# Optimization experiments

Measured on AMD Instinct MI355X. Metric: run time of the kernel, lower is better.

Reference implementation:

```python
import jax, jax.numpy as jnp
import numpy as np

B, S, E, H = 1, 2048, 1024, 16
D = E // H  # head_dim = 64


def setup_inputs() -> dict:
    key = jax.random.key(0)
    ks = jax.random.split(key, 9)
    sd = 0.02
    hidden_states = jax.random.normal(ks[0], (B, S, E), dtype=jnp.float32)
    # causal mask: positions with mask==0 are filled with -inf (per masked_fill_)
    mask = jnp.tril(jnp.ones((1, 1, S, S), dtype=bool))
    Wq = jax.random.normal(ks[1], (E, E), dtype=jnp.float32) * sd
    bq = jax.random.normal(ks[2], (E,), dtype=jnp.float32) * sd
    Wk = jax.random.normal(ks[3], (D, E), dtype=jnp.float32) * sd
    bk = jax.random.normal(ks[4], (D,), dtype=jnp.float32) * sd
    Wv = jax.random.normal(ks[5], (D, E), dtype=jnp.float32) * sd
    bv = jax.random.normal(ks[6], (D,), dtype=jnp.float32) * sd
    Wo = jax.random.normal(ks[7], (E, E), dtype=jnp.float32) * sd
    bo = jax.random.normal(ks[8], (E,), dtype=jnp.float32) * sd
    return {"hidden_states": hidden_states, "mask": mask,
            "Wq": Wq, "bq": bq, "Wk": Wk, "bk": bk,
            "Wv": Wv, "bv": bv, "Wo": Wo, "bo": bo}


def reference(hidden_states, mask, Wq, bq, Wk, bk, Wv, bv, Wo, bo):
    bsz, tgt_len, embed_dim = hidden_states.shape
    # projections (torch Linear: x @ W^T + b)
    q = hidden_states @ Wq.T + bq                       # [B, S, E]
    q = q.reshape(bsz, tgt_len, H, D).transpose(0, 2, 1, 3)  # [B, H, S, D]
    k = hidden_states @ Wk.T + bk                       # [B, S, D] shared single KV head
    v = hidden_states @ Wv.T + bv                       # [B, S, D]
    scaling = jnp.sqrt(jnp.asarray(D, dtype=hidden_states.dtype))
    # QK^T with implicit broadcast of the shared K head (instead of expand)
    scores = jnp.einsum('bhqd,bkd->bhqk', q, k) / scaling   # [B, H, S, S]
    scores = jnp.where(mask, scores, -jnp.inf)
    probs = jax.nn.softmax(scores, axis=-1)             # dropout p=0 -> identity
    attn = jnp.einsum('bhqk,bkd->bhqd', probs, v)       # [B, H, S, D]
    attn = attn.transpose(0, 2, 1, 3).reshape(bsz, tgt_len, H * D)
    return attn @ Wo.T + bo                             # [B, S, E]
```

## Files before the change

### kernel.cpp

```cpp
#include <hip/hip_runtime.h>
#include <hip/hip_bf16.h>

typedef __hip_bfloat16 bf16;
typedef __attribute__((ext_vector_type(8))) short short8;
typedef __attribute__((ext_vector_type(4))) short short4v;
typedef __attribute__((ext_vector_type(4))) float f32x4;

__device__ __forceinline__ short8 ld8(const void* p) { return *(const short8*)p; }
__device__ __forceinline__ short4v ld4(const void* p) { return *(const short4v*)p; }

__device__ __forceinline__ void async_cp16(bf16* lds, const bf16* g) {
    __builtin_amdgcn_global_load_lds(
        (const __attribute__((address_space(1))) unsigned int*)g,
        (__attribute__((address_space(3))) unsigned int*)lds, 16, 0, 0);
}

struct bf4 { bf16 a, b, c, d; };

__global__ void cast_kernel(const float* __restrict__ s0, bf16* __restrict__ d0, int n0_,
                            const float* __restrict__ s1, bf16* __restrict__ d1, int n1_,
                            const float* __restrict__ s2, bf16* __restrict__ d2, int n2_,
                            const float* __restrict__ s3, bf16* __restrict__ d3, int n3_,
                            const float* __restrict__ s4, bf16* __restrict__ d4, int n4_) {
    const float* srcs[5] = {s0, s1, s2, s3, s4};
    bf16* dsts[5] = {d0, d1, d2, d3, d4};
    int ns[5] = {n0_, n1_, n2_, n3_, n4_};
    int stride = gridDim.x * blockDim.x;
    int t0 = blockIdx.x * blockDim.x + threadIdx.x;
#pragma unroll
    for (int a = 0; a < 5; ++a) {
        const float4* src = (const float4*)srcs[a];
        bf4* dst = (bf4*)dsts[a];
        int n4 = ns[a] >> 2;
        for (int i = t0; i < n4; i += stride) {
            float4 v = src[i];
            bf4 o = {__float2bfloat16(v.x), __float2bfloat16(v.y),
                     __float2bfloat16(v.z), __float2bfloat16(v.w)};
            dst[i] = o;
        }
    }
}

#define GEMM_STAGE(dst, src_base, row0, ldk)                                   \
    _Pragma("unroll")                                                          \
    for (int u = 0; u < 4; ++u) {                                              \
        int t = wave * 4 + u;                                                  \
        int row = t * 4 + (lane >> 4);                                         \
        int gsrc = (lane & 15) ^ (row & 15);                                   \
        async_cp16(&dst[t * 4][0], src_base + (size_t)(row0 + row) * ldk + k0 + gsrc * 8); \
    }

__global__ void qkv_proj_kernel(const bf16* __restrict__ A,
                                const bf16* __restrict__ Wq, const bf16* __restrict__ Wk,
                                const bf16* __restrict__ Wv,
                                const float* __restrict__ bq, const float* __restrict__ bk,
                                const float* __restrict__ bv,
                                bf16* __restrict__ qo, bf16* __restrict__ ko,
                                bf16* __restrict__ vto, int M, int K) {
    __shared__ __align__(16) bf16 As[64][128];
    __shared__ __align__(16) bf16 Bs[64][128];
    const int nt = blockIdx.x;
    const bf16* W;
    const float* bias;
    int mode, nw0;
    if (nt < 16)      { W = Wq; bias = bq; mode = 0; nw0 = nt * 64; }
    else if (nt == 16){ W = Wk; bias = bk; mode = 1; nw0 = 0; }
    else              { W = Wv; bias = bv; mode = 2; nw0 = 0; }

    const int tid = threadIdx.x;
    const int wave = tid >> 6, lane = tid & 63;
    const int l16 = lane & 15, quad = lane >> 4;
    const int wr = wave >> 1, wc = wave & 1;
    const int m0 = blockIdx.y * 64;

    f32x4 acc[2][2];
    const f32x4 z = {0.f, 0.f, 0.f, 0.f};
#pragma unroll
    for (int mi = 0; mi < 2; ++mi)
#pragma unroll
        for (int ni = 0; ni < 2; ++ni) acc[mi][ni] = z;

    for (int k0 = 0; k0 < K; k0 += 128) {
        GEMM_STAGE(As, A, m0, K)
        GEMM_STAGE(Bs, W, nw0, K)
        __syncthreads();

        short8 af[2][4], bfr[2][4];
#pragma unroll
        for (int mi = 0; mi < 2; ++mi) {
            int R = wr * 32 + mi * 16 + l16;
#pragma unroll
            for (int kc = 0; kc < 4; ++kc)
                af[mi][kc] = ld8(&As[R][((kc * 4 + quad) ^ (R & 15)) * 8]);
        }
#pragma unroll
        for (int ni = 0; ni < 2; ++ni) {
            int r = wc * 32 + ni * 16 + l16;
#pragma unroll
            for (int kc = 0; kc < 4; ++kc)
                bfr[ni][kc] = ld8(&Bs[r][((kc * 4 + quad) ^ (r & 15)) * 8]);
        }
#pragma unroll
        for (int kc = 0; kc < 4; ++kc)
#pragma unroll
            for (int mi = 0; mi < 2; ++mi)
#pragma unroll
                for (int ni = 0; ni < 2; ++ni)
                    acc[mi][ni] = __builtin_amdgcn_mfma_f32_16x16x32_bf16(
                        af[mi][kc], bfr[ni][kc], acc[mi][ni], 0, 0, 0);
        __syncthreads();
    }

#pragma unroll
    for (int mi = 0; mi < 2; ++mi)
#pragma unroll
        for (int ni = 0; ni < 2; ++ni)
#pragma unroll
            for (int r = 0; r < 4; ++r) {
                int row = m0 + wr * 32 + mi * 16 + quad * 4 + r;
                int c = wc * 32 + ni * 16 + l16;
                float v = acc[mi][ni][r] + bias[nw0 + c];
                if (mode == 0)
                    qo[(size_t)row * 1024 + nt * 64 + c] = __float2bfloat16(v * 0.125f);
                else if (mode == 1)
                    ko[(size_t)row * 64 + c] = __float2bfloat16(v);
                else
                    vto[(size_t)c * M + row] = __float2bfloat16(v);
            }
}

__global__ void gemm_bt_mfma(const bf16* __restrict__ A, const bf16* __restrict__ W,
                             const float* __restrict__ bias, float* __restrict__ C,
                             int M, int N, int K) {
    __shared__ __align__(16) bf16 As[64][128];
    __shared__ __align__(16) bf16 Bs[64][128];
    const int tid = threadIdx.x;
    const int wave = tid >> 6, lane = tid & 63;
    const int l16 = lane & 15, quad = lane >> 4;
    const int wr = wave >> 1, wc = wave & 1;
    const int m0 = blockIdx.y * 64, n0 = blockIdx.x * 64;

    f32x4 acc[2][2];
    const f32x4 z = {0.f, 0.f, 0.f, 0.f};
#pragma unroll
    for (int mi = 0; mi < 2; ++mi)
#pragma unroll
        for (int ni = 0; ni < 2; ++ni) acc[mi][ni] = z;

    for (int k0 = 0; k0 < K; k0 += 128) {
        GEMM_STAGE(As, A, m0, K)
        GEMM_STAGE(Bs, W, n0, K)
        __syncthreads();

        short8 af[2][4], bfr[2][4];
#pragma unroll
        for (int mi = 0; mi < 2; ++mi) {
            int R = wr * 32 + mi * 16 + l16;
#pragma unroll
            for (int kc = 0; kc < 4; ++kc)
                af[mi][kc] = ld8(&As[R][((kc * 4 + quad) ^ (R & 15)) * 8]);
        }
#pragma unroll
        for (int ni = 0; ni < 2; ++ni) {
            int r = wc * 32 + ni * 16 + l16;
#pragma unroll
            for (int kc = 0; kc < 4; ++kc)
                bfr[ni][kc] = ld8(&Bs[r][((kc * 4 + quad) ^ (r & 15)) * 8]);
        }
#pragma unroll
        for (int kc = 0; kc < 4; ++kc)
#pragma unroll
            for (int mi = 0; mi < 2; ++mi)
#pragma unroll
                for (int ni = 0; ni < 2; ++ni)
                    acc[mi][ni] = __builtin_amdgcn_mfma_f32_16x16x32_bf16(
                        af[mi][kc], bfr[ni][kc], acc[mi][ni], 0, 0, 0);
        __syncthreads();
    }

#pragma unroll
    for (int mi = 0; mi < 2; ++mi)
#pragma unroll
        for (int ni = 0; ni < 2; ++ni)
#pragma unroll
            for (int r = 0; r < 4; ++r) {
                int row = m0 + wr * 32 + mi * 16 + quad * 4 + r;
                int col = n0 + wc * 32 + ni * 16 + l16;
                C[(size_t)row * N + col] = acc[mi][ni][r] + bias[col];
            }
}

__global__ void flash_mfma_kernel(const bf16* __restrict__ Q, const bf16* __restrict__ Kg,
                                  const bf16* __restrict__ VT,
                                  bf16* __restrict__ Opart, float* __restrict__ Lpart,
                                  bf16* __restrict__ attn, int S) {
    const int s = blockIdx.x;
    int i, c;
    if (s < 32)      { c = 0; i = s; }
    else if (s < 56) { c = 1; i = s - 24; }
    else if (s < 72) { c = 2; i = s - 40; }
    else             { c = 3; i = s - 48; }

    __shared__ __align__(16) bf16 Ks[64][64];
    __shared__ __align__(16) bf16 Vt[64][64];

    const int h = blockIdx.y;
    const int q0 = i * 64;
    const int tid = threadIdx.x;
    const int wave = tid >> 6, lane = tid & 63;
    const int l16 = lane & 15, quad = lane >> 4;
    const int lr = lane >> 3, lsw = (lane & 7) ^ (lr & 7);
    const int qrow = q0 + wave * 16;

    short8 qf[2];
#pragma unroll
    for (int kc = 0; kc < 2; ++kc)
        qf[kc] = ld8(Q + (size_t)(qrow + l16) * 1024 + h * 64 + kc * 32 + quad * 8);

    f32x4 of[4];
    const f32x4 z = {0.f, 0.f, 0.f, 0.f};
#pragma unroll
    for (int dt = 0; dt < 4; ++dt) of[dt] = z;
    float lsum = 0.f;

    const int jt0 = c * 8;
    const int jt1 = min(c * 8 + 8, i + 1);

    for (int jt = jt0; jt < jt1; ++jt) {
        const int j0 = jt * 64;
#pragma unroll
        for (int u = 0; u < 2; ++u) {
            int t = wave * 2 + u;
            async_cp16(&Ks[t * 8][0], Kg + (size_t)(j0 + t * 8 + lr) * 64 + lsw * 8);
            async_cp16(&Vt[t * 8][0], VT + (size_t)(t * 8 + lr) * S + j0 + lsw * 8);
        }
        __syncthreads();

        f32x4 sc[4];
#pragma unroll
        for (int nt = 0; nt < 4; ++nt) {
            int R = nt * 16 + l16;
            sc[nt] = __builtin_amdgcn_mfma_f32_16x16x32_bf16(
                ld8(&Ks[R][(quad ^ (R & 7)) * 8]), qf[0], z, 0, 0, 0);
            sc[nt] = __builtin_amdgcn_mfma_f32_16x16x32_bf16(
                ld8(&Ks[R][((4 + quad) ^ (R & 7)) * 8]), qf[1], sc[nt], 0, 0, 0);
        }
        if (j0 + 63 > qrow) {
#pragma unroll
            for (int nt = 0; nt < 4; ++nt)
#pragma unroll
                for (int r = 0; r < 4; ++r)
                    if (j0 + nt * 16 + quad * 4 + r > qrow + l16) sc[nt][r] = -1e30f;
        }

        short4v p4[4];
#pragma unroll
        for (int nt = 0; nt < 4; ++nt)
#pragma unroll
            for (int r = 0; r < 4; ++r) {
                bf16 b = __float2bfloat16(__expf(sc[nt][r]));
                lsum += __bfloat162float(b);
                p4[nt][r] = *reinterpret_cast<short*>(&b);
            }

#pragma unroll
        for (int dt = 0; dt < 4; ++dt) {
            int d = dt * 16 + l16;
            int xr = d & 7;
#pragma unroll
            for (int nt = 0; nt < 4; ++nt) {
                int g = 2 * nt + (quad >> 1);
                short4v vf = ld4(&Vt[d][((g ^ xr) * 8) + (quad & 1) * 4]);
                of[dt] = __builtin_amdgcn_mfma_f32_16x16x16bf16_1k(
                    p4[nt], vf, of[dt], 0, 0, 0);
            }
        }
        __syncthreads();
    }

    float Lred = lsum;
    Lred += __shfl_xor(Lred, 16);
    Lred += __shfl_xor(Lred, 32);

    if (s < 8) {
        float inv[4];
#pragma unroll
        for (int r = 0; r < 4; ++r)
            inv[r] = 1.f / __shfl(Lred, quad * 4 + r);
#pragma unroll
        for (int dt = 0; dt < 4; ++dt)
#pragma unroll
            for (int r = 0; r < 4; ++r) {
                int row = q0 + wave * 16 + quad * 4 + r;
                attn[(size_t)row * 1024 + h * 64 + dt * 16 + l16] =
                    __float2bfloat16(of[dt][r] * inv[r]);
            }
        return;
    }

    bf16* Op = Opart + ((size_t)s * 16 + h) * 4096;
#pragma unroll
    for (int dt = 0; dt < 4; ++dt)
#pragma unroll
        for (int r = 0; r < 4; ++r) {
            int row = wave * 16 + quad * 4 + r;
            Op[row * 64 + dt * 16 + l16] = __float2bfloat16(of[dt][r]);
        }
    if (quad == 0) {
        float* L = Lpart + ((size_t)s * 16 + h) * 64;
        L[wave * 16 + l16] = Lred;
    }
}

__global__ void flash_merge_kernel(const bf16* __restrict__ Opart,
                                   const float* __restrict__ Lpart,
                                   bf16* __restrict__ attn) {
    const int i = blockIdx.x + 8, h = blockIdx.y;
    const int nch = (i >> 3) + 1;
    const int tid = threadIdx.x;
    const int row = tid >> 2, cg = (tid & 3) * 16;

    float L = 0.f;
    for (int cc = 0; cc < nch; ++cc) {
        int s = (cc == 0) ? i : (cc == 1) ? 24 + i : (cc == 2) ? 40 + i : 48 + i;
        L += Lpart[((size_t)s * 16 + h) * 64 + row];
    }
    float inv = 1.f / L;

    float o[16];
#pragma unroll
    for (int j = 0; j < 16; ++j) o[j] = 0.f;
    for (int cc = 0; cc < nch; ++cc) {
        int s = (cc == 0) ? i : (cc == 1) ? 24 + i : (cc == 2) ? 40 + i : 48 + i;
        const bf16* Op = Opart + ((size_t)s * 16 + h) * 4096 + row * 64 + cg;
#pragma unroll
        for (int j = 0; j < 16; ++j) o[j] += __bfloat162float(Op[j]);
    }
    bf16* dst = attn + (size_t)(i * 64 + row) * 1024 + h * 64 + cg;
#pragma unroll
    for (int j = 0; j < 16; ++j) dst[j] = __float2bfloat16(o[j] * inv);
}

extern "C" void kernel_launch(void* const* d_in, const int* in_sizes, int n_in,
                              void* d_out, int out_size, void* d_ws, size_t ws_size,
                              hipStream_t stream) {
    const int S = 2048, E = 1024, D = 64;

    const float* hs = (const float*)d_in[0];
    const float* Wq = (const float*)d_in[2];
    const float* bq = (const float*)d_in[3];
    const float* Wk = (const float*)d_in[4];
    const float* bk = (const float*)d_in[5];
    const float* Wv = (const float*)d_in[6];
    const float* bv = (const float*)d_in[7];
    const float* Wo = (const float*)d_in[8];
    const float* bo = (const float*)d_in[9];
    float* out = (float*)d_out;

    bf16* ws = (bf16*)d_ws;
    bf16* hsb = ws;
    bf16* wqb = hsb + (size_t)S * E;
    bf16* wkb = wqb + (size_t)E * E;
    bf16* wvb = wkb + (size_t)D * E;
    bf16* wob = wvb + (size_t)D * E;
    bf16* q = wob + (size_t)E * E;
    bf16* kbuf = q + (size_t)S * E;
    bf16* vt = kbuf + (size_t)S * D;
    bf16* attn = vt + (size_t)S * D;
    bf16* Opart = attn + (size_t)S * E;
    float* Lpart = (float*)(Opart + (size_t)1280 * 4096);

    cast_kernel<<<512, 256, 0, stream>>>(hs, hsb, S * E,
                                         Wq, wqb, E * E,
                                         Wk, wkb, D * E,
                                         Wv, wvb, D * E,
                                         Wo, wob, E * E);
    qkv_proj_kernel<<<dim3(18, S / 64), 256, 0, stream>>>(hsb, wqb, wkb, wvb,
                                                          bq, bk, bv,
                                                          q, kbuf, vt, S, E);
    flash_mfma_kernel<<<dim3(80, 16), 256, 0, stream>>>(q, kbuf, vt, Opart, Lpart, attn, S);
    flash_merge_kernel<<<dim3(24, 16), 256, 0, stream>>>(Opart, Lpart, attn);
    gemm_bt_mfma<<<dim3(E / 64, S / 64), 256, 0, stream>>>(attn, wob, bo, out, S, E, E);
}
```

Before: 138.8 us.

## Split flash attention waves over key columns with register-prefetched K/V

The flash kernel now gives each wave 16 key columns of every 64-key tile instead of 16 query rows. K and V fragments are loaded straight into registers with a one-tile-ahead prefetch, which removes the per-tile LDS staging and the two barriers per iteration. Each wave then keeps partial outputs for all 64 query rows, and these are reduced across waves through LDS atomicAdds into an fp32 scratch buffer before the existing output and partial-write paths. This raises register pressure (launch bounds set to 3 blocks per CU) and adds an LDS atomic reduction at the end of every block.

Measured after the change: 265.3 us. +91.2%, slower.

```diff
diff --git a/kernel.cpp b/kernel.cpp
--- a/kernel.cpp
+++ b/kernel.cpp
@@ -190,10 +190,11 @@
             }
 }
 
-__global__ void flash_mfma_kernel(const bf16* __restrict__ Q, const bf16* __restrict__ Kg,
-                                  const bf16* __restrict__ VT,
-                                  bf16* __restrict__ Opart, float* __restrict__ Lpart,
-                                  bf16* __restrict__ attn, int S) {
+__global__ void __launch_bounds__(256, 3)
+flash_mfma_kernel(const bf16* __restrict__ Q, const bf16* __restrict__ Kg,
+                  const bf16* __restrict__ VT,
+                  bf16* __restrict__ Opart, float* __restrict__ Lpart,
+                  bf16* __restrict__ attn, int S) {
     const int s = blockIdx.x;
     int i, c;
     if (s < 32)      { c = 0; i = s; }
@@ -201,115 +202,128 @@
     else if (s < 72) { c = 2; i = s - 40; }
     else             { c = 3; i = s - 48; }
 
-    __shared__ __align__(16) bf16 Ks[64][64];
-    __shared__ __align__(16) bf16 Vt[64][64];
+    __shared__ float Osum[64][68];
+    __shared__ float Ls[64];
 
     const int h = blockIdx.y;
     const int q0 = i * 64;
     const int tid = threadIdx.x;
-    const int wave = tid >> 6, lane = tid & 63;
+    const int wk = tid >> 6, lane = tid & 63;
     const int l16 = lane & 15, quad = lane >> 4;
-    const int lr = lane >> 3, lsw = (lane & 7) ^ (lr & 7);
-    const int qrow = q0 + wave * 16;
-
-    short8 qf[2];
-#pragma unroll
-    for (int kc = 0; kc < 2; ++kc)
-        qf[kc] = ld8(Q + (size_t)(qrow + l16) * 1024 + h * 64 + kc * 32 + quad * 8);
-
-    f32x4 of[4];
+
+    for (int j = tid; j < 64 * 68; j += 256) (&Osum[0][0])[j] = 0.f;
+    if (tid < 64) Ls[tid] = 0.f;
+
+    short8 qfr[4][2];
+#pragma unroll
+    for (int qt = 0; qt < 4; ++qt)
+#pragma unroll
+        for (int dc = 0; dc < 2; ++dc)
+            qfr[qt][dc] = ld8(Q + (size_t)(q0 + qt * 16 + l16) * 1024 + h * 64
+                                + dc * 32 + quad * 8);
+
+    f32x4 of[4][4];
     const f32x4 z = {0.f, 0.f, 0.f, 0.f};
 #pragma unroll
-    for (int dt = 0; dt < 4; ++dt) of[dt] = z;
-    float lsum = 0.f;
+    for (int qt = 0; qt < 4; ++qt)
+#pragma unroll
+        for (int dt = 0; dt < 4; ++dt) of[qt][dt] = z;
+    float lsum[4] = {0.f, 0.f, 0.f, 0.f};
 
     const int jt0 = c * 8;
     const int jt1 = min(c * 8 + 8, i + 1);
 
+    const bf16* kbase = Kg + (size_t)(wk * 16 + l16) * 64 + quad * 8;
+    const bf16* vbase = VT + (size_t)l16 * S + wk * 16 + quad * 4;
+
+    short8  kc0 = ld8(kbase + (size_t)jt0 * 4096);
+    short8  kc1 = ld8(kbase + (size_t)jt0 * 4096 + 32);
+    short4v vc0 = ld4(vbase + jt0 * 64);
+    short4v vc1 = ld4(vbase + (size_t)16 * S + jt0 * 64);
+    short4v vc2 = ld4(vbase + (size_t)32 * S + jt0 * 64);
+    short4v vc3 = ld4(vbase + (size_t)48 * S + jt0 * 64);
+
     for (int jt = jt0; jt < jt1; ++jt) {
         const int j0 = jt * 64;
-#pragma unroll
-        for (int u = 0; u < 2; ++u) {
-            int t = wave * 2 + u;
-            async_cp16(&Ks[t * 8][0], Kg + (size_t)(j0 + t * 8 + lr) * 64 + lsw * 8);
-            async_cp16(&Vt[t * 8][0], VT + (size_t)(t * 8 + lr) * S + j0 + lsw * 8);
-        }
-        __syncthreads();
+        const bool more = (jt + 1 < jt1);
+        short8 kn0, kn1; short4v vn0, vn1, vn2, vn3;
+        if (more) {
+            kn0 = ld8(kbase + (size_t)(jt + 1) * 4096);
+            kn1 = ld8(kbase + (size_t)(jt + 1) * 4096 + 32);
+            vn0 = ld4(vbase + (jt + 1) * 64);
+            vn1 = ld4(vbase + (size_t)16 * S + (jt + 1) * 64);
+            vn2 = ld4(vbase + (size_t)32 * S + (jt + 1) * 64);
+            vn3 = ld4(vbase + (size_t)48 * S + (jt + 1) * 64);
+        }
 
         f32x4 sc[4];
 #pragma unroll
-        for (int nt = 0; nt < 4; ++nt) {
-            int R = nt * 16 + l16;
-            sc[nt] = __builtin_amdgcn_mfma_f32_16x16x32_bf16(
-                ld8(&Ks[R][(quad ^ (R & 7)) * 8]), qf[0], z, 0, 0, 0);
-            sc[nt] = __builtin_amdgcn_mfma_f32_16x16x32_bf16(
-                ld8(&Ks[R][((4 + quad) ^ (R & 7)) * 8]), qf[1], sc[nt], 0, 0, 0);
-        }
-        if (j0 + 63 > qrow) {
-#pragma unroll
-            for (int nt = 0; nt < 4; ++nt)
+        for (int qt = 0; qt < 4; ++qt) {
+            sc[qt] = __builtin_amdgcn_mfma_f32_16x16x32_bf16(kc0, qfr[qt][0], z, 0, 0, 0);
+            sc[qt] = __builtin_amdgcn_mfma_f32_16x16x32_bf16(kc1, qfr[qt][1], sc[qt], 0, 0, 0);
+        }
+
+        const int kg = j0 + wk * 16 + quad * 4;
+#pragma unroll
+        for (int qt = 0; qt < 4; ++qt) {
+            if (j0 + wk * 16 + 15 > q0 + qt * 16) {
 #pragma unroll
                 for (int r = 0; r < 4; ++r)
-                    if (j0 + nt * 16 + quad * 4 + r > qrow + l16) sc[nt][r] = -1e30f;
+                    if (kg + r > q0 + qt * 16 + l16) sc[qt][r] = -1e30f;
+            }
         }
 
         short4v p4[4];
 #pragma unroll
-        for (int nt = 0; nt < 4; ++nt)
+        for (int qt = 0; qt < 4; ++qt)
 #pragma unroll
             for (int r = 0; r < 4; ++r) {
-                bf16 b = __float2bfloat16(__expf(sc[nt][r]));
-                lsum += __bfloat162float(b);
-                p4[nt][r] = *reinterpret_cast<short*>(&b);
+                bf16 b = __float2bfloat16(__expf(sc[qt][r]));
+                lsum[qt] += __bfloat162float(b);
+                p4[qt][r] = *reinterpret_cast<short*>(&b);
             }
 
 #pragma unroll
-        for (int dt = 0; dt < 4; ++dt) {
-            int d = dt * 16 + l16;
-            int xr = d & 7;
-#pragma unroll
-            for (int nt = 0; nt < 4; ++nt) {
-                int g = 2 * nt + (quad >> 1);
-                short4v vf = ld4(&Vt[d][((g ^ xr) * 8) + (quad & 1) * 4]);
-                of[dt] = __builtin_amdgcn_mfma_f32_16x16x16bf16_1k(
-                    p4[nt], vf, of[dt], 0, 0, 0);
-            }
-        }
-        __syncthreads();
-    }
-
-    float Lred = lsum;
-    Lred += __shfl_xor(Lred, 16);
-    Lred += __shfl_xor(Lred, 32);
-
+        for (int qt = 0; qt < 4; ++qt) {
+            of[qt][0] = __builtin_amdgcn_mfma_f32_16x16x16bf16_1k(p4[qt], vc0, of[qt][0], 0, 0, 0);
+            of[qt][1] = __builtin_amdgcn_mfma_f32_16x16x16bf16_1k(p4[qt], vc1, of[qt][1], 0, 0, 0);
+            of[qt][2] = __builtin_amdgcn_mfma_f32_16x16x16bf16_1k(p4[qt], vc2, of[qt][2], 0, 0, 0);
+            of[qt][3] = __builtin_amdgcn_mfma_f32_16x16x16bf16_1k(p4[qt], vc3, of[qt][3], 0, 0, 0);
+        }
+
+        if (more) { kc0 = kn0; kc1 = kn1; vc0 = vn0; vc1 = vn1; vc2 = vn2; vc3 = vn3; }
+    }
+
+    __syncthreads();
+
+#pragma unroll
+    for (int qt = 0; qt < 4; ++qt)
+#pragma unroll
+        for (int dt = 0; dt < 4; ++dt)
+#pragma unroll
+            for (int r = 0; r < 4; ++r)
+                atomicAdd(&Osum[qt * 16 + quad * 4 + r][dt * 16 + l16], of[qt][dt][r]);
+#pragma unroll
+    for (int qt = 0; qt < 4; ++qt)
+        atomicAdd(&Ls[qt * 16 + l16], lsum[qt]);
+    __syncthreads();
+
+    const int row = tid >> 2, cg = (tid & 3) * 16;
     if (s < 8) {
-        float inv[4];
-#pragma unroll
-        for (int r = 0; r < 4; ++r)
-            inv[r] = 1.f / __shfl(Lred, quad * 4 + r);
-#pragma unroll
-        for (int dt = 0; dt < 4; ++dt)
-#pragma unroll
-            for (int r = 0; r < 4; ++r) {
-                int row = q0 + wave * 16 + quad * 4 + r;
-                attn[(size_t)row * 1024 + h * 64 + dt * 16 + l16] =
-                    __float2bfloat16(of[dt][r] * inv[r]);
-            }
+        float inv = 1.f / Ls[row];
+        bf16* dst = attn + (size_t)(q0 + row) * 1024 + h * 64 + cg;
+#pragma unroll
+        for (int j = 0; j < 16; ++j)
+            dst[j] = __float2bfloat16(Osum[row][cg + j] * inv);
         return;
     }
 
-    bf16* Op = Opart + ((size_t)s * 16 + h) * 4096;
-#pragma unroll
-    for (int dt = 0; dt < 4; ++dt)
-#pragma unroll
-        for (int r = 0; r < 4; ++r) {
-            int row = wave * 16 + quad * 4 + r;
-            Op[row * 64 + dt * 16 + l16] = __float2bfloat16(of[dt][r]);
-        }
-    if (quad == 0) {
-        float* L = Lpart + ((size_t)s * 16 + h) * 64;
-        L[wave * 16 + l16] = Lred;
-    }
+    bf16* Op = Opart + ((size_t)s * 16 + h) * 4096 + row * 64 + cg;
+#pragma unroll
+    for (int j = 0; j < 16; ++j)
+        Op[j] = __float2bfloat16(Osum[row][cg + j]);
+    if ((tid & 3) == 0)
+        Lpart[((size_t)s * 16 + h) * 64 + row] = Ls[row];
 }
 
 __global__ void flash_merge_kernel(const bf16* __restrict__ Opart,
```

## Process two query heads per block to reuse shared K/V tiles

Applied to the files above, without the earlier changes.

Each flash-attention block now handles two heads at once. It loads the shared single-head K and V tiles into LDS and registers once, then runs both heads' QK^T, softmax and PV MFMAs from them. This halves the grid and the redundant K/V global and LDS traffic for the multi-query layout. In exchange, per-thread register use grows (two accumulator sets, cached K/V fragments), which is capped with launch bounds, and fewer blocks means less parallelism.

New measurement: 145.3 us. +4.7%, slower.

```diff
diff --git a/kernel.cpp b/kernel.cpp
--- a/kernel.cpp
+++ b/kernel.cpp
@@ -190,10 +190,11 @@
             }
 }
 
-__global__ void flash_mfma_kernel(const bf16* __restrict__ Q, const bf16* __restrict__ Kg,
-                                  const bf16* __restrict__ VT,
-                                  bf16* __restrict__ Opart, float* __restrict__ Lpart,
-                                  bf16* __restrict__ attn, int S) {
+__global__ void __launch_bounds__(256, 2)
+flash_mfma_kernel(const bf16* __restrict__ Q, const bf16* __restrict__ Kg,
+                  const bf16* __restrict__ VT,
+                  bf16* __restrict__ Opart, float* __restrict__ Lpart,
+                  bf16* __restrict__ attn, int S) {
     const int s = blockIdx.x;
     int i, c;
     if (s < 32)      { c = 0; i = s; }
@@ -204,7 +205,7 @@
     __shared__ __align__(16) bf16 Ks[64][64];
     __shared__ __align__(16) bf16 Vt[64][64];
 
-    const int h = blockIdx.y;
+    const int h0 = blockIdx.y * 2;
     const int q0 = i * 64;
     const int tid = threadIdx.x;
     const int wave = tid >> 6, lane = tid & 63;
@@ -212,16 +213,21 @@
     const int lr = lane >> 3, lsw = (lane & 7) ^ (lr & 7);
     const int qrow = q0 + wave * 16;
 
-    short8 qf[2];
-#pragma unroll
-    for (int kc = 0; kc < 2; ++kc)
-        qf[kc] = ld8(Q + (size_t)(qrow + l16) * 1024 + h * 64 + kc * 32 + quad * 8);
-
-    f32x4 of[4];
+    short8 qf[2][2];
+#pragma unroll
+    for (int hh = 0; hh < 2; ++hh)
+#pragma unroll
+        for (int kc = 0; kc < 2; ++kc)
+            qf[hh][kc] = ld8(Q + (size_t)(qrow + l16) * 1024 + (h0 + hh) * 64
+                               + kc * 32 + quad * 8);
+
+    f32x4 of[2][4];
     const f32x4 z = {0.f, 0.f, 0.f, 0.f};
 #pragma unroll
-    for (int dt = 0; dt < 4; ++dt) of[dt] = z;
-    float lsum = 0.f;
+    for (int hh = 0; hh < 2; ++hh)
+#pragma unroll
+        for (int dt = 0; dt < 4; ++dt) of[hh][dt] = z;
+    float lsum[2] = {0.f, 0.f};
 
     const int jt0 = c * 8;
     const int jt1 = min(c * 8 + 8, i + 1);
@@ -236,33 +242,14 @@
         }
         __syncthreads();
 
-        f32x4 sc[4];
+        short8 kf[4][2];
 #pragma unroll
         for (int nt = 0; nt < 4; ++nt) {
             int R = nt * 16 + l16;
-            sc[nt] = __builtin_amdgcn_mfma_f32_16x16x32_bf16(
-                ld8(&Ks[R][(quad ^ (R & 7)) * 8]), qf[0], z, 0, 0, 0);
-            sc[nt] = __builtin_amdgcn_mfma_f32_16x16x32_bf16(
-                ld8(&Ks[R][((4 + quad) ^ (R & 7)) * 8]), qf[1], sc[nt], 0, 0, 0);
-        }
-        if (j0 + 63 > qrow) {
-#pragma unroll
-            for (int nt = 0; nt < 4; ++nt)
-#pragma unroll
-                for (int r = 0; r < 4; ++r)
-                    if (j0 + nt * 16 + quad * 4 + r > qrow + l16) sc[nt][r] = -1e30f;
-        }
-
-        short4v p4[4];
-#pragma unroll
-        for (int nt = 0; nt < 4; ++nt)
-#pragma unroll
-            for (int r = 0; r < 4; ++r) {
-                bf16 b = __float2bfloat16(__expf(sc[nt][r]));
-                lsum += __bfloat162float(b);
-                p4[nt][r] = *reinterpret_cast<short*>(&b);
-            }
-
+            kf[nt][0] = ld8(&Ks[R][(quad ^ (R & 7)) * 8]);
+            kf[nt][1] = ld8(&Ks[R][((4 + quad) ^ (R & 7)) * 8]);
+        }
+        short4v vf[4][4];
 #pragma unroll
         for (int dt = 0; dt < 4; ++dt) {
             int d = dt * 16 + l16;
@@ -270,45 +257,89 @@
 #pragma unroll
             for (int nt = 0; nt < 4; ++nt) {
                 int g = 2 * nt + (quad >> 1);
-                short4v vf = ld4(&Vt[d][((g ^ xr) * 8) + (quad & 1) * 4]);
-                of[dt] = __builtin_amdgcn_mfma_f32_16x16x16bf16_1k(
-                    p4[nt], vf, of[dt], 0, 0, 0);
-            }
-        }
-        __syncthreads();
-    }
-
-    float Lred = lsum;
-    Lred += __shfl_xor(Lred, 16);
-    Lred += __shfl_xor(Lred, 32);
+                vf[dt][nt] = ld4(&Vt[d][((g ^ xr) * 8) + (quad & 1) * 4]);
+            }
+        }
+
+#pragma unroll
+        for (int hh = 0; hh < 2; ++hh) {
+            f32x4 sc[4];
+#pragma unroll
+            for (int nt = 0; nt < 4; ++nt) {
+                sc[nt] = __builtin_amdgcn_mfma_f32_16x16x32_bf16(
+                    kf[nt][0], qf[hh][0], z, 0, 0, 0);
+                sc[nt] = __builtin_amdgcn_mfma_f32_16x16x32_bf16(
+                    kf[nt][1], qf[hh][1], sc[nt], 0, 0, 0);
+            }
+            if (j0 + 63 > qrow) {
+#pragma unroll
+                for (int nt = 0; nt < 4; ++nt)
+#pragma unroll
+                    for (int r = 0; r < 4; ++r)
+                        if (j0 + nt * 16 + quad * 4 + r > qrow + l16)
+                            sc[nt][r] = -1e30f;
+            }
+
+            short4v p4[4];
+#pragma unroll
+            for (int nt = 0; nt < 4; ++nt)
+#pragma unroll
+                for (int r = 0; r < 4; ++r) {
+                    bf16 b = __float2bfloat16(__expf(sc[nt][r]));
+                    lsum[hh] += __bfloat162float(b);
+                    p4[nt][r] = *reinterpret_cast<short*>(&b);
+                }
+
+#pragma unroll
+            for (int dt = 0; dt < 4; ++dt)
+#pragma unroll
+                for (int nt = 0; nt < 4; ++nt)
+                    of[hh][dt] = __builtin_amdgcn_mfma_f32_16x16x16bf16_1k(
+                        p4[nt], vf[dt][nt], of[hh][dt], 0, 0, 0);
+        }
+        __syncthreads();
+    }
+
+    float Lred[2];
+#pragma unroll
+    for (int hh = 0; hh < 2; ++hh) {
+        float t = lsum[hh];
+        t += __shfl_xor(t, 16);
+        t += __shfl_xor(t, 32);
+        Lred[hh] = t;
+    }
 
     if (s < 8) {
-        float inv[4];
-#pragma unroll
-        for (int r = 0; r < 4; ++r)
-            inv[r] = 1.f / __shfl(Lred, quad * 4 + r);
+#pragma unroll
+        for (int hh = 0; hh < 2; ++hh) {
+            float inv[4];
+#pragma unroll
+            for (int r = 0; r < 4; ++r)
+                inv[r] = 1.f / __shfl(Lred[hh], quad * 4 + r);
+#pragma unroll
+            for (int dt = 0; dt < 4; ++dt)
+#pragma unroll
+                for (int r = 0; r < 4; ++r) {
+                    int row = q0 + wave * 16 + quad * 4 + r;
+                    attn[(size_t)row * 1024 + (h0 + hh) * 64 + dt * 16 + l16] =
+                        __float2bfloat16(of[hh][dt][r] * inv[r]);
+                }
+        }
+        return;
+    }
+
+#pragma unroll
+    for (int hh = 0; hh < 2; ++hh) {
+        bf16* Op = Opart + ((size_t)s * 16 + h0 + hh) * 4096;
 #pragma unroll
         for (int dt = 0; dt < 4; ++dt)
 #pragma unroll
             for (int r = 0; r < 4; ++r) {
-                int row = q0 + wave * 16 + quad * 4 + r;
-                attn[(size_t)row * 1024 + h * 64 + dt * 16 + l16] =
-                    __float2bfloat16(of[dt][r] * inv[r]);
-            }
-        return;
-    }
-
-    bf16* Op = Opart + ((size_t)s * 16 + h) * 4096;
-#pragma unroll
-    for (int dt = 0; dt < 4; ++dt)
-#pragma unroll
-        for (int r = 0; r < 4; ++r) {
-            int row = wave * 16 + quad * 4 + r;
-            Op[row * 64 + dt * 16 + l16] = __float2bfloat16(of[dt][r]);
-        }
-    if (quad == 0) {
-        float* L = Lpart + ((size_t)s * 16 + h) * 64;
-        L[wave * 16 + l16] = Lred;
+                int row = wave * 16 + quad * 4 + r;
+                Op[row * 64 + dt * 16 + l16] = __float2bfloat16(of[hh][dt][r]);
+            }
+        if (quad == 0)
+            Lpart[((size_t)s * 16 + h0 + hh) * 64 + wave * 16 + l16] = Lred[hh];
     }
 }
 
@@ -378,7 +409,7 @@
     qkv_proj_kernel<<<dim3(18, S / 64), 256, 0, stream>>>(hsb, wqb, wkb, wvb,
                                                           bq, bk, bv,
                                                           q, kbuf, vt, S, E);
-    flash_mfma_kernel<<<dim3(80, 16), 256, 0, stream>>>(q, kbuf, vt, Opart, Lpart, attn, S);
+    flash_mfma_kernel<<<dim3(80, 8), 256, 0, stream>>>(q, kbuf, vt, Opart, Lpart, attn, S);
     flash_merge_kernel<<<dim3(24, 16), 256, 0, stream>>>(Opart, Lpart, attn);
     gemm_bt_mfma<<<dim3(E / 64, S / 64), 256, 0, stream>>>(attn, wob, bo, out, S, E, E);
 }
```

## Fuse split-KV merge into flash kernel via last-block atomic counter

Applied to the files above, without the earlier changes.

Removes the separate flash_merge_kernel launch. Each split block of the flash kernel increments a per-(query tile, head) atomic counter after writing its partials, and the block that finishes last merges them into attn. The counters are zeroed inside the existing cast kernel, so no extra launch is needed for that. This saves one kernel launch and its tail gap, at the cost of thread fences and an atomic per block.

Result: slower. 316.4 us (+128.0%).

```diff
diff --git a/kernel.cpp b/kernel.cpp
--- a/kernel.cpp
+++ b/kernel.cpp
@@ -21,12 +21,14 @@
                             const float* __restrict__ s1, bf16* __restrict__ d1, int n1_,
                             const float* __restrict__ s2, bf16* __restrict__ d2, int n2_,
                             const float* __restrict__ s3, bf16* __restrict__ d3, int n3_,
-                            const float* __restrict__ s4, bf16* __restrict__ d4, int n4_) {
+                            const float* __restrict__ s4, bf16* __restrict__ d4, int n4_,
+                            int* __restrict__ cnt, int ncnt) {
     const float* srcs[5] = {s0, s1, s2, s3, s4};
     bf16* dsts[5] = {d0, d1, d2, d3, d4};
     int ns[5] = {n0_, n1_, n2_, n3_, n4_};
     int stride = gridDim.x * blockDim.x;
     int t0 = blockIdx.x * blockDim.x + threadIdx.x;
+    if (t0 < ncnt) cnt[t0] = 0;
 #pragma unroll
     for (int a = 0; a < 5; ++a) {
         const float4* src = (const float4*)srcs[a];
@@ -193,7 +195,7 @@
 __global__ void flash_mfma_kernel(const bf16* __restrict__ Q, const bf16* __restrict__ Kg,
                                   const bf16* __restrict__ VT,
                                   bf16* __restrict__ Opart, float* __restrict__ Lpart,
-                                  bf16* __restrict__ attn, int S) {
+                                  bf16* __restrict__ attn, int* __restrict__ cnt, int S) {
     const int s = blockIdx.x;
     int i, c;
     if (s < 32)      { c = 0; i = s; }
@@ -203,6 +205,7 @@
 
     __shared__ __align__(16) bf16 Ks[64][64];
     __shared__ __align__(16) bf16 Vt[64][64];
+    __shared__ int lastflag;
 
     const int h = blockIdx.y;
     const int q0 = i * 64;
@@ -310,20 +313,22 @@
         float* L = Lpart + ((size_t)s * 16 + h) * 64;
         L[wave * 16 + l16] = Lred;
     }
-}
-
-__global__ void flash_merge_kernel(const bf16* __restrict__ Opart,
-                                   const float* __restrict__ Lpart,
-                                   bf16* __restrict__ attn) {
-    const int i = blockIdx.x + 8, h = blockIdx.y;
+
     const int nch = (i >> 3) + 1;
-    const int tid = threadIdx.x;
+    __threadfence();
+    if (tid == 0) {
+        int old = atomicAdd(&cnt[(i - 8) * 16 + h], 1);
+        lastflag = (old == nch - 1) ? 1 : 0;
+    }
+    __syncthreads();
+    if (!lastflag) return;
+    __threadfence();
+
     const int row = tid >> 2, cg = (tid & 3) * 16;
-
     float L = 0.f;
     for (int cc = 0; cc < nch; ++cc) {
-        int s = (cc == 0) ? i : (cc == 1) ? 24 + i : (cc == 2) ? 40 + i : 48 + i;
-        L += Lpart[((size_t)s * 16 + h) * 64 + row];
+        int ss = (cc == 0) ? i : (cc == 1) ? 24 + i : (cc == 2) ? 40 + i : 48 + i;
+        L += Lpart[((size_t)ss * 16 + h) * 64 + row];
     }
     float inv = 1.f / L;
 
@@ -331,12 +336,12 @@
 #pragma unroll
     for (int j = 0; j < 16; ++j) o[j] = 0.f;
     for (int cc = 0; cc < nch; ++cc) {
-        int s = (cc == 0) ? i : (cc == 1) ? 24 + i : (cc == 2) ? 40 + i : 48 + i;
-        const bf16* Op = Opart + ((size_t)s * 16 + h) * 4096 + row * 64 + cg;
-#pragma unroll
-        for (int j = 0; j < 16; ++j) o[j] += __bfloat162float(Op[j]);
-    }
-    bf16* dst = attn + (size_t)(i * 64 + row) * 1024 + h * 64 + cg;
+        int ss = (cc == 0) ? i : (cc == 1) ? 24 + i : (cc == 2) ? 40 + i : 48 + i;
+        const bf16* Op2 = Opart + ((size_t)ss * 16 + h) * 4096 + row * 64 + cg;
+#pragma unroll
+        for (int j = 0; j < 16; ++j) o[j] += __bfloat162float(Op2[j]);
+    }
+    bf16* dst = attn + (size_t)(q0 + row) * 1024 + h * 64 + cg;
 #pragma unroll
     for (int j = 0; j < 16; ++j) dst[j] = __float2bfloat16(o[j] * inv);
 }
@@ -369,16 +374,18 @@
     bf16* attn = vt + (size_t)S * D;
     bf16* Opart = attn + (size_t)S * E;
     float* Lpart = (float*)(Opart + (size_t)1280 * 4096);
+    int* cnt = (int*)(Lpart + (size_t)1280 * 64);
 
     cast_kernel<<<512, 256, 0, stream>>>(hs, hsb, S * E,
                                          Wq, wqb, E * E,
                                          Wk, wkb, D * E,
                                          Wv, wvb, D * E,
-                                         Wo, wob, E * E);
+                                         Wo, wob, E * E,
+                                         cnt, 24 * 16);
     qkv_proj_kernel<<<dim3(18, S / 64), 256, 0, stream>>>(hsb, wqb, wkb, wvb,
                                                           bq, bk, bv,
                                                           q, kbuf, vt, S, E);
-    flash_mfma_kernel<<<dim3(80, 16), 256, 0, stream>>>(q, kbuf, vt, Opart, Lpart, attn, S);
-    flash_merge_kernel<<<dim3(24, 16), 256, 0, stream>>>(Opart, Lpart, attn);
+    flash_mfma_kernel<<<dim3(80, 16), 256, 0, stream>>>(q, kbuf, vt, Opart, Lpart,
+                                                        attn, cnt, S);
     gemm_bt_mfma<<<dim3(E / 64, S / 64), 256, 0, stream>>>(attn, wob, bo, out, S, E, E);
 }
```
